# Optimization experiments

Hardware: AMD Instinct MI355X
Metric: run time of the kernel (lower is better)

Reference implementation:

```python
import jax, jax.numpy as jnp
import numpy as np

N = 10000
E = 320000
F_IN = 256
HID = 64
HEADS = 8
NUM_CLASSES = 2
NEG_SLOPE = 0.2


def _glorot(key, shape):
    fan_in, fan_out = shape[0], shape[-1]
    lim = (6.0 / (fan_in + fan_out)) ** 0.5
    return jax.random.uniform(key, shape, jnp.float32, -lim, lim)


def setup_inputs() -> dict:
    key = jax.random.key(0)
    ks = jax.random.split(key, 20)
    x = jax.random.normal(ks[0], (N, F_IN), jnp.float32)
    edge_index = jax.random.randint(ks[1], (2, E), 0, N, jnp.int64)
    d = {
        "x": x,
        "edge_index": edge_index,
        # layer 1: in=256 -> heads=8, C=64, concat -> 512
        "W1": _glorot(ks[2], (F_IN, HEADS * HID)),
        "a_src1": _glorot(ks[3], (HEADS, HID)),
        "a_dst1": _glorot(ks[4], (HEADS, HID)),
        "b1": jnp.zeros((HEADS * HID,), jnp.float32),
        # layer 2: in=512 -> heads=8, C=64, concat -> 512
        "W2": _glorot(ks[5], (HEADS * HID, HEADS * HID)),
        "a_src2": _glorot(ks[6], (HEADS, HID)),
        "a_dst2": _glorot(ks[7], (HEADS, HID)),
        "b2": jnp.zeros((HEADS * HID,), jnp.float32),
        # output conv: in=512 -> heads=1, C=64, no concat
        "W3": _glorot(ks[8], (HEADS * HID, HID)),
        "a_src3": _glorot(ks[9], (1, HID)),
        "a_dst3": _glorot(ks[10], (1, HID)),
        "b3": jnp.zeros((HID,), jnp.float32),
        # classifier
        "lin_W": _glorot(ks[11], (HID, NUM_CLASSES)),
        "lin_b": jnp.zeros((NUM_CLASSES,), jnp.float32),
    }
    return d


def _gat_layer(x, src, dst, W, a_src, a_dst, b, heads, ch, concat):
    # project: [N, H, C]
    h = (x @ W).reshape(-1, heads, ch)
    alpha_src = jnp.sum(h * a_src, axis=-1)  # [N, H]
    alpha_dst = jnp.sum(h * a_dst, axis=-1)  # [N, H]
    # per-edge attention logits (edge j -> i uses src alpha of j, dst alpha of i)
    e = jax.nn.leaky_relu(alpha_src[src] + alpha_dst[dst], NEG_SLOPE)  # [E, H]
    # segment softmax over incoming edges of each destination node
    m = jax.ops.segment_max(e, dst, num_segments=N)  # [N, H]
    m = jnp.where(jnp.isfinite(m), m, 0.0)
    ex = jnp.exp(e - m[dst])
    denom = jax.ops.segment_sum(ex, dst, num_segments=N)
    alpha = ex / (denom[dst] + 1e-16)  # [E, H]
    # weighted message aggregation
    out = jax.ops.segment_sum(h[src] * alpha[:, :, None], dst, num_segments=N)  # [N, H, C]
    if concat:
        out = out.reshape(N, heads * ch)
    else:
        out = out.mean(axis=1)
    return out + b


def reference(x, edge_index, W1, a_src1, a_dst1, b1, W2, a_src2, a_dst2, b2,
              W3, a_src3, a_dst3, b3, lin_W, lin_b):
    # PyG GATConv adds self loops by default
    loop = jnp.arange(N, dtype=edge_index.dtype)
    src = jnp.concatenate([edge_index[0], loop])
    dst = jnp.concatenate([edge_index[1], loop])

    h = _gat_layer(x, src, dst, W1, a_src1, a_dst1, b1, HEADS, HID, True)
    h = jax.nn.elu(h)
    h = _gat_layer(h, src, dst, W2, a_src2, a_dst2, b2, HEADS, HID, True)
    h = jax.nn.elu(h)
    h = _gat_layer(h, src, dst, W3, a_src3, a_dst3, b3, 1, HID, False)
    logits = h @ lin_W + lin_b
    return jax.nn.log_softmax(logits, axis=1)
```

## Files before the change

kernel.cpp:

```cpp
#include <hip/hip_runtime.h>
#include <cmath>

#define NEG 0.2f

typedef __bf16 bf16x8 __attribute__((ext_vector_type(8)));
typedef float  f32x4  __attribute__((ext_vector_type(4)));

__device__ __forceinline__ void async16(const __bf16* g, __bf16* l) {
  __builtin_amdgcn_global_load_lds(
      (const __attribute__((address_space(1))) void*)g,
      (__attribute__((address_space(3))) void*)l, 16, 0, 0);
}
__device__ __forceinline__ f32x4 mfma16(bf16x8 a, bf16x8 b, f32x4 c) {
  return __builtin_amdgcn_mfma_f32_16x16x32_bf16(a, b, c, 0, 0, 0);
}

__global__ void count_kernel(const int* __restrict__ ei, int* __restrict__ counts, int E, int Nn) {
  int e = blockIdx.x * blockDim.x + threadIdx.x;
  if (e >= E + Nn) return;
  int d = (e < E) ? ei[E + e] : (e - E);
  atomicAdd(&counts[d], 1);
}

__global__ __launch_bounds__(1024) void scan_kernel(const int* __restrict__ counts,
                                                    int* __restrict__ row_ptr,
                                                    int* __restrict__ cursor,
                                                    int n, int total) {
  __shared__ int sums[1024];
  int t = threadIdx.x;
  int per = (n + 1023) >> 10;
  int base = t * per;
  int s = 0;
  for (int i = 0; i < per; ++i) { int idx = base + i; if (idx < n) s += counts[idx]; }
  sums[t] = s;
  __syncthreads();
  for (int st = 1; st < 1024; st <<= 1) {
    int v = (t >= st) ? sums[t - st] : 0;
    __syncthreads();
    sums[t] += v;
    __syncthreads();
  }
  int off = (t == 0) ? 0 : sums[t - 1];
  for (int i = 0; i < per; ++i) {
    int idx = base + i;
    if (idx < n) { row_ptr[idx] = off; cursor[idx] = off; off += counts[idx]; }
  }
  if (t == 0) row_ptr[n] = total;
}

__global__ void scatter_kernel(const int* __restrict__ ei, int* __restrict__ cursor,
                               int* __restrict__ src_sorted, int E, int Nn) {
  int e = blockIdx.x * blockDim.x + threadIdx.x;
  if (e >= E + Nn) return;
  int s, d;
  if (e < E) { s = ei[e]; d = ei[E + e]; } else { s = e - E; d = e - E; }
  int pos = atomicAdd(&cursor[d], 1);
  src_sorted[pos] = s;
}

__global__ void prep_kernel(const float* __restrict__ x, __bf16* __restrict__ xsh,
                            __bf16* __restrict__ xsl,
                            const float* __restrict__ W1, __bf16* __restrict__ W1th,
                            __bf16* __restrict__ W1tl,
                            const float* __restrict__ W2, __bf16* __restrict__ W2th,
                            __bf16* __restrict__ W2tl,
                            const float* __restrict__ W3, __bf16* __restrict__ W3th,
                            __bf16* __restrict__ W3tl,
                            int* __restrict__ counts, int Nn) {
  int i = blockIdx.x * blockDim.x + threadIdx.x;
  if (i < Nn) { counts[i] = 0; return; }
  i -= Nn;
  int nx = Nn * 256;
  if (i < nx) {
    float v = x[i];
    __bf16 h = (__bf16)v;
    xsh[i] = h;
    xsl[i] = (__bf16)(v - (float)h);
    return;
  }
  i -= nx;
  if (i < 256 * 512) {
    int k = i / 512, c = i % 512;
    float v = W1[i];
    __bf16 h = (__bf16)v;
    W1th[(size_t)c * 256 + k] = h;
    W1tl[(size_t)c * 256 + k] = (__bf16)(v - (float)h);
    return;
  }
  i -= 256 * 512;
  if (i < 512 * 512) {
    int k = i / 512, c = i % 512;
    float v = W2[i];
    __bf16 h = (__bf16)v;
    W2th[(size_t)c * 512 + k] = h;
    W2tl[(size_t)c * 512 + k] = (__bf16)(v - (float)h);
    return;
  }
  i -= 512 * 512;
  if (i < 512 * 64) {
    int k = i / 64, c = i % 64;
    float v = W3[i];
    __bf16 h = (__bf16)v;
    W3th[(size_t)c * 512 + k] = h;
    W3tl[(size_t)c * 512 + k] = (__bf16)(v - (float)h);
    return;
  }
}

template <bool BF16OUT, bool SWZ>
__global__ __launch_bounds__(256, 3) void gemm_v2(
    const __bf16* __restrict__ Ah, const __bf16* __restrict__ Al,
    const __bf16* __restrict__ Bth, const __bf16* __restrict__ Btl,
    __bf16* __restrict__ Cb, float* __restrict__ Cf,
    const float* __restrict__ asrc, const float* __restrict__ adst,
    float* __restrict__ als, float* __restrict__ ald,
    int M, int K, int Nc, int PX, int hstride) {
  __shared__ __bf16 sAh[128 * 64], sAl[128 * 64], sBh[64 * 64], sBl[64 * 64];

  int x, y;
  if (SWZ) {
    int p = blockIdx.x;
    int c = p & 7, j = p >> 3;
    x = c * PX + (j >> 3);
    y = j & 7;
  } else {
    x = blockIdx.x;
    y = 0;
  }
  int rowBase = x * 128, colBase = y * 64;
  if (rowBase >= M) return;

  int tid = threadIdx.x;
  int lane = tid & 63, wave = tid >> 6;
  int r16 = lane & 15, koct = lane >> 4, msk = r16 & 7;

  f32x4 acc[2][4] = {};

  for (int k0 = 0; k0 < K; k0 += 64) {
    __syncthreads();
#pragma unroll
    for (int r = 0; r < 4; ++r) {
      int flat = r * 256 + tid;
      int row = flat >> 3;
      int grow = rowBase + row;
      if (grow >= M) grow = M - 1;
      int s = (flat & 7) ^ (row & 7);
      size_t go = (size_t)grow * K + k0 + s * 8;
      int lb = (r * 256 + wave * 64) * 8;
      async16(Ah + go, sAh + lb);
      async16(Al + go, sAl + lb);
    }
#pragma unroll
    for (int r = 0; r < 2; ++r) {
      int flat = r * 256 + tid;
      int col = flat >> 3;
      int s = (flat & 7) ^ (col & 7);
      size_t go = (size_t)(colBase + col) * K + k0 + s * 8;
      int lb = (r * 256 + wave * 64) * 8;
      async16(Bth + go, sBh + lb);
      async16(Btl + go, sBl + lb);
    }
    __syncthreads();

#pragma unroll
    for (int kk = 0; kk < 2; ++kk) {
      bf16x8 ah[2], al[2], bh[4], bl[4];
#pragma unroll
      for (int fm = 0; fm < 2; ++fm) {
        int off = (wave * 32 + fm * 16 + r16) * 64 + (((kk * 4 + koct) ^ msk) * 8);
        ah[fm] = *reinterpret_cast<const bf16x8*>(sAh + off);
        al[fm] = *reinterpret_cast<const bf16x8*>(sAl + off);
      }
#pragma unroll
      for (int fn = 0; fn < 4; ++fn) {
        int off = (fn * 16 + r16) * 64 + (((kk * 4 + koct) ^ msk) * 8);
        bh[fn] = *reinterpret_cast<const bf16x8*>(sBh + off);
        bl[fn] = *reinterpret_cast<const bf16x8*>(sBl + off);
      }
#pragma unroll
      for (int fm = 0; fm < 2; ++fm)
#pragma unroll
        for (int fn = 0; fn < 4; ++fn) {
          acc[fm][fn] = mfma16(ah[fm], bh[fn], acc[fm][fn]);
          acc[fm][fn] = mfma16(al[fm], bh[fn], acc[fm][fn]);
          acc[fm][fn] = mfma16(ah[fm], bl[fn], acc[fm][fn]);
        }
    }
  }

  int head = y;
  float asv[4], adv[4];
#pragma unroll
  for (int fn = 0; fn < 4; ++fn) {
    asv[fn] = asrc[head * 64 + fn * 16 + r16];
    adv[fn] = adst[head * 64 + fn * 16 + r16];
  }
#pragma unroll
  for (int fm = 0; fm < 2; ++fm)
#pragma unroll
    for (int r = 0; r < 4; ++r) {
      int row = rowBase + wave * 32 + fm * 16 + koct * 4 + r;
      float ps = 0.f, pd = 0.f;
#pragma unroll
      for (int fn = 0; fn < 4; ++fn) {
        float v = acc[fm][fn][r];
        ps = fmaf(v, asv[fn], ps);
        pd = fmaf(v, adv[fn], pd);
        if (row < M) {
          int col = colBase + fn * 16 + r16;
          if (BF16OUT) Cb[(size_t)row * Nc + col] = (__bf16)v;
          else         Cf[(size_t)row * Nc + col] = v;
        }
      }
#pragma unroll
      for (int sft = 1; sft < 16; sft <<= 1) {
        ps += __shfl_xor(ps, sft);
        pd += __shfl_xor(pd, sft);
      }
      if (r16 == 0 && row < M) {
        als[(size_t)row * hstride + head] = ps;
        ald[(size_t)row * hstride + head] = pd;
      }
    }
}

__global__ __launch_bounds__(256) void agg8_kernel(const __bf16* __restrict__ Hb,
                                                   const float* __restrict__ als,
                                                   const float* __restrict__ ald,
                                                   const float* __restrict__ bias,
                                                   const int* __restrict__ row_ptr,
                                                   const int* __restrict__ src_sorted,
                                                   __bf16* __restrict__ Oh,
                                                   __bf16* __restrict__ Ol,
                                                   int Nn) {
  int n = (blockIdx.x * 256 + threadIdx.x) >> 6;
  if (n >= Nn) return;
  int lane = threadIdx.x & 63;
  int hh = lane >> 3;
  int start = row_ptr[n], deg = row_ptr[n + 1] - start;
  float aldn = ald[n * 8 + hh];

  float pm = -INFINITY;
  for (int e = (lane >> 3); e < deg; e += 8)
    pm = fmaxf(pm, als[src_sorted[start + e] * 8 + (lane & 7)]);
  pm = fmaxf(pm, __shfl_xor(pm, 8));
  pm = fmaxf(pm, __shfl_xor(pm, 16));
  pm = fmaxf(pm, __shfl_xor(pm, 32));
  float m = __shfl(pm, hh) + aldn;
  m = m > 0.f ? m : NEG * m;

  float acc[8] = {};
  float ssum = 0.f;
  const __bf16* hcol = Hb + lane * 8;
  for (int e0 = 0; e0 < deg; e0 += 4) {
    int idx[4];
    float av[4];
    bf16x8 v[4];
#pragma unroll
    for (int i = 0; i < 4; ++i) {
      int e = e0 + i;
      if (e > deg - 1) e = deg - 1;
      idx[i] = src_sorted[start + e];
    }
#pragma unroll
    for (int i = 0; i < 4; ++i) av[i] = als[idx[i] * 8 + hh];
#pragma unroll
    for (int i = 0; i < 4; ++i)
      v[i] = *reinterpret_cast<const bf16x8*>(hcol + (size_t)idx[i] * 512);
#pragma unroll
    for (int i = 0; i < 4; ++i) {
      float l = av[i] + aldn;
      l = l > 0.f ? l : NEG * l;
      float w = (e0 + i < deg) ? expf(l - m) : 0.f;
      ssum += w;
#pragma unroll
      for (int j = 0; j < 8; ++j) acc[j] = fmaf(w, (float)v[i][j], acc[j]);
    }
  }

  float inv = 1.f / (ssum + 1e-16f);
  bf16x8 vh, vl;
#pragma unroll
  for (int j = 0; j < 8; ++j) {
    float v = acc[j] * inv + bias[lane * 8 + j];
    v = v > 0.f ? v : expm1f(v);
    __bf16 h = (__bf16)v;
    vh[j] = h;
    vl[j] = (__bf16)(v - (float)h);
  }
  *reinterpret_cast<bf16x8*>(Oh + (size_t)n * 512 + lane * 8) = vh;
  *reinterpret_cast<bf16x8*>(Ol + (size_t)n * 512 + lane * 8) = vl;
}

__global__ __launch_bounds__(256) void agg1cls_kernel(const float* __restrict__ Hf,
                                                      const float* __restrict__ als,
                                                      const float* __restrict__ ald,
                                                      const float* __restrict__ bias,
                                                      const int* __restrict__ row_ptr,
                                                      const int* __restrict__ src_sorted,
                                                      const float* __restrict__ lw,
                                                      const float* __restrict__ lb,
                                                      float* __restrict__ out,
                                                      int Nn) {
  int n = (blockIdx.x * 256 + threadIdx.x) >> 6;
  if (n >= Nn) return;
  int lane = threadIdx.x & 63;
  int start = row_ptr[n], deg = row_ptr[n + 1] - start;
  float aldn = ald[n];

  float pm = -INFINITY;
  for (int e = lane; e < deg; e += 64) pm = fmaxf(pm, als[src_sorted[start + e]]);
  for (int s = 32; s; s >>= 1) pm = fmaxf(pm, __shfl_xor(pm, s));
  float m = pm + aldn;
  m = m > 0.f ? m : NEG * m;

  float acc = 0.f, ssum = 0.f;
  for (int e0 = 0; e0 < deg; e0 += 4) {
    int idx[4];
    float av[4], hv[4];
#pragma unroll
    for (int i = 0; i < 4; ++i) {
      int e = e0 + i;
      if (e > deg - 1) e = deg - 1;
      idx[i] = src_sorted[start + e];
    }
#pragma unroll
    for (int i = 0; i < 4; ++i) av[i] = als[idx[i]];
#pragma unroll
    for (int i = 0; i < 4; ++i) hv[i] = Hf[(size_t)idx[i] * 64 + lane];
#pragma unroll
    for (int i = 0; i < 4; ++i) {
      float l = av[i] + aldn;
      l = l > 0.f ? l : NEG * l;
      float w = (e0 + i < deg) ? expf(l - m) : 0.f;
      ssum += w;
      acc = fmaf(w, hv[i], acc);
    }
  }
  float o = acc / (ssum + 1e-16f) + bias[lane];

  float p0 = o * lw[lane * 2 + 0];
  float p1 = o * lw[lane * 2 + 1];
  for (int s = 32; s; s >>= 1) {
    p0 += __shfl_xor(p0, s);
    p1 += __shfl_xor(p1, s);
  }
  if (lane == 0) {
    p0 += lb[0];
    p1 += lb[1];
    float mx = fmaxf(p0, p1);
    float lse = mx + logf(expf(p0 - mx) + expf(p1 - mx));
    out[n * 2 + 0] = p0 - lse;
    out[n * 2 + 1] = p1 - lse;
  }
}

extern "C" void kernel_launch(void* const* d_in, const int* in_sizes, int n_in,
                              void* d_out, int out_size, void* d_ws, size_t ws_size,
                              hipStream_t stream) {
  (void)n_in; (void)out_size; (void)ws_size;
  const float* x     = (const float*)d_in[0];
  const int*   ei    = (const int*)d_in[1];
  const float* W1    = (const float*)d_in[2];
  const float* asrc1 = (const float*)d_in[3];
  const float* adst1 = (const float*)d_in[4];
  const float* b1    = (const float*)d_in[5];
  const float* W2    = (const float*)d_in[6];
  const float* asrc2 = (const float*)d_in[7];
  const float* adst2 = (const float*)d_in[8];
  const float* b2    = (const float*)d_in[9];
  const float* W3    = (const float*)d_in[10];
  const float* asrc3 = (const float*)d_in[11];
  const float* adst3 = (const float*)d_in[12];
  const float* b3    = (const float*)d_in[13];
  const float* linW  = (const float*)d_in[14];
  const float* linb  = (const float*)d_in[15];
  float* out = (float*)d_out;

  int Nn = in_sizes[0] / 256;
  int E  = in_sizes[1] / 2;
  int E2 = E + Nn;

  char* w = (char*)d_ws;
  auto carve = [&](size_t bytes) {
    char* p = w;
    w += (bytes + 63) & ~(size_t)63;
    return p;
  };
  __bf16* xsh  = (__bf16*)carve((size_t)Nn * 256 * 2);
  __bf16* xsl  = (__bf16*)carve((size_t)Nn * 256 * 2);
  __bf16* Ahb  = (__bf16*)carve((size_t)Nn * 512 * 2);
  __bf16* Alb  = (__bf16*)carve((size_t)Nn * 512 * 2);
  __bf16* Hb16 = (__bf16*)carve((size_t)Nn * 512 * 2);
  float*  Hb3  = (float*)carve((size_t)Nn * 64 * 4);
  float*  als  = (float*)carve((size_t)Nn * 8 * 4);
  float*  ald  = (float*)carve((size_t)Nn * 8 * 4);
  __bf16* W1th = (__bf16*)carve(256 * 512 * 2);
  __bf16* W1tl = (__bf16*)carve(256 * 512 * 2);
  __bf16* W2th = (__bf16*)carve(512 * 512 * 2);
  __bf16* W2tl = (__bf16*)carve(512 * 512 * 2);
  __bf16* W3th = (__bf16*)carve(512 * 64 * 2);
  __bf16* W3tl = (__bf16*)carve(512 * 64 * 2);
  int* counts     = (int*)carve((size_t)Nn * 4);
  int* cursor     = (int*)carve((size_t)Nn * 4);
  int* row_ptr    = (int*)carve(((size_t)Nn + 1) * 4);
  int* src_sorted = (int*)carve((size_t)E2 * 4);

  int prep_total = Nn + Nn * 256 + 256 * 512 + 512 * 512 + 512 * 64;
  prep_kernel<<<(prep_total + 255) / 256, 256, 0, stream>>>(
      x, xsh, xsl, W1, W1th, W1tl, W2, W2th, W2tl, W3, W3th, W3tl, counts, Nn);
  count_kernel<<<(E2 + 255) / 256, 256, 0, stream>>>(ei, counts, E, Nn);
  scan_kernel<<<1, 1024, 0, stream>>>(counts, row_ptr, cursor, Nn, E2);
  scatter_kernel<<<(E2 + 255) / 256, 256, 0, stream>>>(ei, cursor, src_sorted, E, Nn);

  int gx = (Nn + 127) / 128;
  int PX = (gx + 7) / 8;
  int nblk = 64 * PX;
  int ga = (Nn + 3) / 4;

  gemm_v2<true, true><<<nblk, 256, 0, stream>>>(xsh, xsl, W1th, W1tl, Hb16, nullptr,
                                                asrc1, adst1, als, ald, Nn, 256, 512, PX, 8);
  agg8_kernel<<<ga, 256, 0, stream>>>(Hb16, als, ald, b1, row_ptr, src_sorted, Ahb, Alb, Nn);
  gemm_v2<true, true><<<nblk, 256, 0, stream>>>(Ahb, Alb, W2th, W2tl, Hb16, nullptr,
                                                asrc2, adst2, als, ald, Nn, 512, 512, PX, 8);
  agg8_kernel<<<ga, 256, 0, stream>>>(Hb16, als, ald, b2, row_ptr, src_sorted, Ahb, Alb, Nn);
  gemm_v2<false, false><<<gx, 256, 0, stream>>>(Ahb, Alb, W3th, W3tl, nullptr, Hb3,
                                                asrc3, adst3, als, ald, Nn, 512, 64, 0, 1);
  agg1cls_kernel<<<ga, 256, 0, stream>>>(Hb3, als, ald, b3, row_ptr, src_sorted,
                                         linW, linb, out, Nn);
}
```

Before: 245.7 us.

## Drop weight low-part split and use single-pass online softmax in aggregation

Weights are now converted to a single bf16 copy, so the GEMM loads one B tile and issues two MFMAs per fragment instead of three. Shared memory shrinks, and the occupancy hint goes from 3 to 4 blocks. The aggregation kernels drop the separate max pass over neighbours. They use a lazily rescaled online softmax over chunks of 8 edges with fast __expf. The cost is reduced weight precision, and accuracy relies on the rescale threshold keeping the exponentials bounded.

```diff
diff --git a/kernel.cpp b/kernel.cpp
--- a/kernel.cpp
+++ b/kernel.cpp
@@ -61,11 +61,8 @@
 __global__ void prep_kernel(const float* __restrict__ x, __bf16* __restrict__ xsh,
                             __bf16* __restrict__ xsl,
                             const float* __restrict__ W1, __bf16* __restrict__ W1th,
-                            __bf16* __restrict__ W1tl,
                             const float* __restrict__ W2, __bf16* __restrict__ W2th,
-                            __bf16* __restrict__ W2tl,
                             const float* __restrict__ W3, __bf16* __restrict__ W3th,
-                            __bf16* __restrict__ W3tl,
                             int* __restrict__ counts, int Nn) {
   int i = blockIdx.x * blockDim.x + threadIdx.x;
   if (i < Nn) { counts[i] = 0; return; }
@@ -81,41 +78,32 @@
   i -= nx;
   if (i < 256 * 512) {
     int k = i / 512, c = i % 512;
-    float v = W1[i];
-    __bf16 h = (__bf16)v;
-    W1th[(size_t)c * 256 + k] = h;
-    W1tl[(size_t)c * 256 + k] = (__bf16)(v - (float)h);
+    W1th[(size_t)c * 256 + k] = (__bf16)W1[i];
     return;
   }
   i -= 256 * 512;
   if (i < 512 * 512) {
     int k = i / 512, c = i % 512;
-    float v = W2[i];
-    __bf16 h = (__bf16)v;
-    W2th[(size_t)c * 512 + k] = h;
-    W2tl[(size_t)c * 512 + k] = (__bf16)(v - (float)h);
+    W2th[(size_t)c * 512 + k] = (__bf16)W2[i];
     return;
   }
   i -= 512 * 512;
   if (i < 512 * 64) {
     int k = i / 64, c = i % 64;
-    float v = W3[i];
-    __bf16 h = (__bf16)v;
-    W3th[(size_t)c * 512 + k] = h;
-    W3tl[(size_t)c * 512 + k] = (__bf16)(v - (float)h);
+    W3th[(size_t)c * 512 + k] = (__bf16)W3[i];
     return;
   }
 }
 
 template <bool BF16OUT, bool SWZ>
-__global__ __launch_bounds__(256, 3) void gemm_v2(
+__global__ __launch_bounds__(256, 4) void gemm_v2(
     const __bf16* __restrict__ Ah, const __bf16* __restrict__ Al,
-    const __bf16* __restrict__ Bth, const __bf16* __restrict__ Btl,
+    const __bf16* __restrict__ Bth,
     __bf16* __restrict__ Cb, float* __restrict__ Cf,
     const float* __restrict__ asrc, const float* __restrict__ adst,
     float* __restrict__ als, float* __restrict__ ald,
     int M, int K, int Nc, int PX, int hstride) {
-  __shared__ __bf16 sAh[128 * 64], sAl[128 * 64], sBh[64 * 64], sBl[64 * 64];
+  __shared__ __bf16 sAh[128 * 64], sAl[128 * 64], sBh[64 * 64];
 
   int x, y;
   if (SWZ) {
@@ -158,13 +146,12 @@
       size_t go = (size_t)(colBase + col) * K + k0 + s * 8;
       int lb = (r * 256 + wave * 64) * 8;
       async16(Bth + go, sBh + lb);
-      async16(Btl + go, sBl + lb);
     }
     __syncthreads();
 
 #pragma unroll
     for (int kk = 0; kk < 2; ++kk) {
-      bf16x8 ah[2], al[2], bh[4], bl[4];
+      bf16x8 ah[2], al[2], bh[4];
 #pragma unroll
       for (int fm = 0; fm < 2; ++fm) {
         int off = (wave * 32 + fm * 16 + r16) * 64 + (((kk * 4 + koct) ^ msk) * 8);
@@ -175,7 +162,6 @@
       for (int fn = 0; fn < 4; ++fn) {
         int off = (fn * 16 + r16) * 64 + (((kk * 4 + koct) ^ msk) * 8);
         bh[fn] = *reinterpret_cast<const bf16x8*>(sBh + off);
-        bl[fn] = *reinterpret_cast<const bf16x8*>(sBl + off);
       }
 #pragma unroll
       for (int fm = 0; fm < 2; ++fm)
@@ -183,7 +169,6 @@
         for (int fn = 0; fn < 4; ++fn) {
           acc[fm][fn] = mfma16(ah[fm], bh[fn], acc[fm][fn]);
           acc[fm][fn] = mfma16(al[fm], bh[fn], acc[fm][fn]);
-          acc[fm][fn] = mfma16(ah[fm], bl[fn], acc[fm][fn]);
         }
     }
   }
@@ -240,38 +225,43 @@
   int start = row_ptr[n], deg = row_ptr[n + 1] - start;
   float aldn = ald[n * 8 + hh];
 
-  float pm = -INFINITY;
-  for (int e = (lane >> 3); e < deg; e += 8)
-    pm = fmaxf(pm, als[src_sorted[start + e] * 8 + (lane & 7)]);
-  pm = fmaxf(pm, __shfl_xor(pm, 8));
-  pm = fmaxf(pm, __shfl_xor(pm, 16));
-  pm = fmaxf(pm, __shfl_xor(pm, 32));
-  float m = __shfl(pm, hh) + aldn;
-  m = m > 0.f ? m : NEG * m;
-
   float acc[8] = {};
   float ssum = 0.f;
+  float mrun = 0.f;
   const __bf16* hcol = Hb + lane * 8;
-  for (int e0 = 0; e0 < deg; e0 += 4) {
-    int idx[4];
-    float av[4];
-    bf16x8 v[4];
-#pragma unroll
-    for (int i = 0; i < 4; ++i) {
+  for (int e0 = 0; e0 < deg; e0 += 8) {
+    int idx[8];
+    float lv[8];
+    bf16x8 v[8];
+#pragma unroll
+    for (int i = 0; i < 8; ++i) {
       int e = e0 + i;
       if (e > deg - 1) e = deg - 1;
       idx[i] = src_sorted[start + e];
     }
 #pragma unroll
-    for (int i = 0; i < 4; ++i) av[i] = als[idx[i] * 8 + hh];
-#pragma unroll
-    for (int i = 0; i < 4; ++i)
+    for (int i = 0; i < 8; ++i) lv[i] = als[idx[i] * 8 + hh];
+#pragma unroll
+    for (int i = 0; i < 8; ++i)
       v[i] = *reinterpret_cast<const bf16x8*>(hcol + (size_t)idx[i] * 512);
-#pragma unroll
-    for (int i = 0; i < 4; ++i) {
-      float l = av[i] + aldn;
+    float lm = -INFINITY;
+#pragma unroll
+    for (int i = 0; i < 8; ++i) {
+      float l = lv[i] + aldn;
       l = l > 0.f ? l : NEG * l;
-      float w = (e0 + i < deg) ? expf(l - m) : 0.f;
+      lv[i] = l;
+      lm = fmaxf(lm, l);
+    }
+    if (__builtin_expect(lm > mrun + 24.f, 0)) {
+      float sc = __expf(mrun - lm);
+      ssum *= sc;
+#pragma unroll
+      for (int j = 0; j < 8; ++j) acc[j] *= sc;
+      mrun = lm;
+    }
+#pragma unroll
+    for (int i = 0; i < 8; ++i) {
+      float w = (e0 + i < deg) ? __expf(lv[i] - mrun) : 0.f;
       ssum += w;
 #pragma unroll
       for (int j = 0; j < 8; ++j) acc[j] = fmaf(w, (float)v[i][j], acc[j]);
@@ -308,31 +298,37 @@
   int start = row_ptr[n], deg = row_ptr[n + 1] - start;
   float aldn = ald[n];
 
-  float pm = -INFINITY;
-  for (int e = lane; e < deg; e += 64) pm = fmaxf(pm, als[src_sorted[start + e]]);
-  for (int s = 32; s; s >>= 1) pm = fmaxf(pm, __shfl_xor(pm, s));
-  float m = pm + aldn;
-  m = m > 0.f ? m : NEG * m;
-
-  float acc = 0.f, ssum = 0.f;
-  for (int e0 = 0; e0 < deg; e0 += 4) {
-    int idx[4];
-    float av[4], hv[4];
-#pragma unroll
-    for (int i = 0; i < 4; ++i) {
+  float acc = 0.f, ssum = 0.f, mrun = 0.f;
+  for (int e0 = 0; e0 < deg; e0 += 8) {
+    int idx[8];
+    float lv[8], hv[8];
+#pragma unroll
+    for (int i = 0; i < 8; ++i) {
       int e = e0 + i;
       if (e > deg - 1) e = deg - 1;
       idx[i] = src_sorted[start + e];
     }
 #pragma unroll
-    for (int i = 0; i < 4; ++i) av[i] = als[idx[i]];
-#pragma unroll
-    for (int i = 0; i < 4; ++i) hv[i] = Hf[(size_t)idx[i] * 64 + lane];
-#pragma unroll
-    for (int i = 0; i < 4; ++i) {
-      float l = av[i] + aldn;
+    for (int i = 0; i < 8; ++i) lv[i] = als[idx[i]];
+#pragma unroll
+    for (int i = 0; i < 8; ++i) hv[i] = Hf[(size_t)idx[i] * 64 + lane];
+    float lm = -INFINITY;
+#pragma unroll
+    for (int i = 0; i < 8; ++i) {
+      float l = lv[i] + aldn;
       l = l > 0.f ? l : NEG * l;
-      float w = (e0 + i < deg) ? expf(l - m) : 0.f;
+      lv[i] = l;
+      lm = fmaxf(lm, l);
+    }
+    if (__builtin_expect(lm > mrun + 24.f, 0)) {
+      float sc = __expf(mrun - lm);
+      ssum *= sc;
+      acc *= sc;
+      mrun = lm;
+    }
+#pragma unroll
+    for (int i = 0; i < 8; ++i) {
+      float w = (e0 + i < deg) ? __expf(lv[i] - mrun) : 0.f;
       ssum += w;
       acc = fmaf(w, hv[i], acc);
     }
@@ -396,11 +392,8 @@
   float*  als  = (float*)carve((size_t)Nn * 8 * 4);
   float*  ald  = (float*)carve((size_t)Nn * 8 * 4);
   __bf16* W1th = (__bf16*)carve(256 * 512 * 2);
-  __bf16* W1tl = (__bf16*)carve(256 * 512 * 2);
   __bf16* W2th = (__bf16*)carve(512 * 512 * 2);
-  __bf16* W2tl = (__bf16*)carve(512 * 512 * 2);
   __bf16* W3th = (__bf16*)carve(512 * 64 * 2);
-  __bf16* W3tl = (__bf16*)carve(512 * 64 * 2);
   int* counts     = (int*)carve((size_t)Nn * 4);
   int* cursor     = (int*)carve((size_t)Nn * 4);
   int* row_ptr    = (int*)carve(((size_t)Nn + 1) * 4);
@@ -408,7 +401,7 @@
 
   int prep_total = Nn + Nn * 256 + 256 * 512 + 512 * 512 + 512 * 64;
   prep_kernel<<<(prep_total + 255) / 256, 256, 0, stream>>>(
-      x, xsh, xsl, W1, W1th, W1tl, W2, W2th, W2tl, W3, W3th, W3tl, counts, Nn);
+      x, xsh, xsl, W1, W1th, W2, W2th, W3, W3th, counts, Nn);
   count_kernel<<<(E2 + 255) / 256, 256, 0, stream>>>(ei, counts, E, Nn);
   scan_kernel<<<1, 1024, 0, stream>>>(counts, row_ptr, cursor, Nn, E2);
   scatter_kernel<<<(E2 + 255) / 256, 256, 0, stream>>>(ei, cursor, src_sorted, E, Nn);
@@ -418,13 +411,13 @@
   int nblk = 64 * PX;
   int ga = (Nn + 3) / 4;
 
-  gemm_v2<true, true><<<nblk, 256, 0, stream>>>(xsh, xsl, W1th, W1tl, Hb16, nullptr,
+  gemm_v2<true, true><<<nblk, 256, 0, stream>>>(xsh, xsl, W1th, Hb16, nullptr,
                                                 asrc1, adst1, als, ald, Nn, 256, 512, PX, 8);
   agg8_kernel<<<ga, 256, 0, stream>>>(Hb16, als, ald, b1, row_ptr, src_sorted, Ahb, Alb, Nn);
-  gemm_v2<true, true><<<nblk, 256, 0, stream>>>(Ahb, Alb, W2th, W2tl, Hb16, nullptr,
+  gemm_v2<true, true><<<nblk, 256, 0, stream>>>(Ahb, Alb, W2th, Hb16, nullptr,
                                                 asrc2, adst2, als, ald, Nn, 512, 512, PX, 8);
   agg8_kernel<<<ga, 256, 0, stream>>>(Hb16, als, ald, b2, row_ptr, src_sorted, Ahb, Alb, Nn);
-  gemm_v2<false, false><<<gx, 256, 0, stream>>>(Ahb, Alb, W3th, W3tl, nullptr, Hb3,
+  gemm_v2<false, false><<<gx, 256, 0, stream>>>(Ahb, Alb, W3th, nullptr, Hb3,
                                                 asrc3, adst3, als, ald, Nn, 512, 64, 0, 1);
   agg1cls_kernel<<<ga, 256, 0, stream>>>(Hb3, als, ald, b3, row_ptr, src_sorted,
                                          linW, linb, out, Nn);
```

After: 215.5 us. 12.3% less time.
